# Performance work log

Hardware: AMD Instinct MI355X
Metric: run time of the kernel (lower is better)

Reference implementation:

```python
import jax, jax.numpy as jnp
import numpy as np


def setup_inputs() -> dict:
    key = jax.random.key(0)
    k1, k2, k3, k4, k5 = jax.random.split(key, 5)
    B, S, D, H, E = 4, 4096, 1024, 1024, 8  # H = per-expert hidden (fuel_dim)
    std = 0.02
    return {
        "hidden_states": jax.random.normal(k1, (B, S, D), dtype=jnp.float32),
        "gate_w": jax.random.normal(k2, (D, E), dtype=jnp.float32) * std,
        "gw": jax.random.normal(k3, (E, D, H), dtype=jnp.float32) * std,
        "pw": jax.random.normal(k4, (E, D, H), dtype=jnp.float32) * std,
        "ow": jax.random.normal(k5, (E, H, D), dtype=jnp.float32) * std,
        "top_k": 2,
    }


def reference(hidden_states, gate_w, gw, pw, ow, top_k):
    B, S, D = hidden_states.shape
    E = gate_w.shape[1]
    x = hidden_states.reshape(-1, D)  # [T, D]
    T = x.shape[0]

    # Router
    router_logits = x @ gate_w  # [T, E]
    routing_probs = jax.nn.softmax(router_logits.astype(jnp.float32), axis=-1)
    top_w, top_i = jax.lax.top_k(routing_probs, top_k)  # [T, k]
    top_w = top_w / jnp.sum(top_w, axis=-1, keepdims=True)
    top_w = top_w.astype(x.dtype)

    # Dense combine weights: zero for unselected experts -> same math as
    # the torch gather/expert/scatter loop.
    combine = jnp.zeros((T, E), dtype=x.dtype).at[
        jnp.arange(T)[:, None], top_i
    ].set(top_w)  # [T, E]

    # SwiGLU experts, batched over the expert dim.
    g = jnp.einsum('td,edh->eth', x, gw)          # [E, T, H]
    p = jnp.einsum('td,edh->eth', x, pw)          # [E, T, H]
    h = g * jax.nn.silu(p)                        # [E, T, H]
    y = jnp.einsum('eth,ehd->etd', h, ow)         # [E, T, D]
    final = jnp.einsum('etd,te->td', y, combine)  # [T, D]
    final = final.reshape(B, S, D)

    # Load-balancing loss (recomputes softmax/topk as the torch fn does)
    expert_mask = jax.nn.one_hot(top_i, E, dtype=jnp.float32)  # [T, k, E]
    tokens_per_expert = jnp.mean(expert_mask, axis=0)          # [k, E]
    router_prob_per_expert = jnp.mean(routing_probs, axis=0)   # [E]
    bl_loss = jnp.sum(tokens_per_expert * router_prob_per_expert[None, :]) * E

    return final, router_logits, bl_loss
```

## Files before the change

kernel.cpp:

```cpp
#include <hip/hip_runtime.h>
#include <hip/hip_bf16.h>
#include <cstdint>

#define T_TOK 16384
#define DDIM  1024

typedef __attribute__((ext_vector_type(8))) short bf16x8;
typedef __attribute__((ext_vector_type(4))) float f32x4;

__device__ __forceinline__ unsigned short f2bf(float f) {
  unsigned u = __builtin_bit_cast(unsigned, f);
  return (unsigned short)((u + 0x7fffu + ((u >> 16) & 1u)) >> 16);
}
__device__ __forceinline__ unsigned pk2(float a, float b) {
  return (unsigned)f2bf(a) | ((unsigned)f2bf(b) << 16);
}
__device__ __forceinline__ void gload16(const void* g, void* l) {
  typedef __attribute__((address_space(1))) const unsigned int gu32;
  typedef __attribute__((address_space(3))) unsigned int lu32;
  __builtin_amdgcn_global_load_lds((gu32*)g, (lu32*)l, 16, 0, 0);
}

__global__ __launch_bounds__(256) void convert_k(
    const float* __restrict__ gw, const float* __restrict__ pw,
    const float* __restrict__ ow, char* __restrict__ wg,
    char* __restrict__ wp, char* __restrict__ wo) {
  __shared__ float t[64][65];
  const int z = blockIdx.z;
  const int arr = z >> 3, e = z & 7;
  const float* src = (arr == 0 ? gw : arr == 1 ? pw : ow) + ((long)e << 20);
  char* dst = (arr == 0 ? wg : arr == 1 ? wp : wo) + ((long)e << 21);
  const int r0 = blockIdx.x * 64, c0 = blockIdx.y * 64;
  const int row = threadIdx.x >> 2, q = threadIdx.x & 3;
  const float4* sp = (const float4*)(src + (long)(r0 + row) * 1024 + c0 + q * 16);
  float4 v0 = sp[0], v1 = sp[1], v2 = sp[2], v3 = sp[3];
  float* tr = &t[row][q * 16];
  tr[0]=v0.x; tr[1]=v0.y; tr[2]=v0.z; tr[3]=v0.w;
  tr[4]=v1.x; tr[5]=v1.y; tr[6]=v1.z; tr[7]=v1.w;
  tr[8]=v2.x; tr[9]=v2.y; tr[10]=v2.z; tr[11]=v2.w;
  tr[12]=v3.x; tr[13]=v3.y; tr[14]=v3.z; tr[15]=v3.w;
  __syncthreads();
  const int cl = row, rq = q;
  uint4 o0, o1;
  o0.x = pk2(t[rq*16+ 0][cl], t[rq*16+ 1][cl]);
  o0.y = pk2(t[rq*16+ 2][cl], t[rq*16+ 3][cl]);
  o0.z = pk2(t[rq*16+ 4][cl], t[rq*16+ 5][cl]);
  o0.w = pk2(t[rq*16+ 6][cl], t[rq*16+ 7][cl]);
  o1.x = pk2(t[rq*16+ 8][cl], t[rq*16+ 9][cl]);
  o1.y = pk2(t[rq*16+10][cl], t[rq*16+11][cl]);
  o1.z = pk2(t[rq*16+12][cl], t[rq*16+13][cl]);
  o1.w = pk2(t[rq*16+14][cl], t[rq*16+15][cl]);
  char* dp = dst + (long)(c0 + cl) * 2048 + (long)(r0 + rq * 16) * 2;
  *(uint4*)dp = o0;
  *(uint4*)(dp + 16) = o1;
}

__global__ __launch_bounds__(256) void router_k(
    const float* __restrict__ x, const float* __restrict__ gatew,
    float* __restrict__ logitsOut, float4* __restrict__ route,
    float* __restrict__ accum, unsigned short* __restrict__ xbo) {
  __shared__ float accB[16];
  const int tid = threadIdx.x;
  if (tid < 16) accB[tid] = 0.f;
  __syncthreads();
  const int lane = tid & 63;
  const int gwave = blockIdx.x * 4 + (tid >> 6);

  for (int g = gwave; g < 4096; g += 1024) {
    const int t0 = g * 4;
    float s[4][8];
#pragma unroll
    for (int tt = 0; tt < 4; ++tt)
#pragma unroll
      for (int e = 0; e < 8; ++e) s[tt][e] = 0.f;

    for (int i = 0; i < 16; ++i) {
      int d = lane + i * 64;
      float4 w0 = *(const float4*)(gatew + d * 8);
      float4 w1 = *(const float4*)(gatew + d * 8 + 4);
#pragma unroll
      for (int tt = 0; tt < 4; ++tt) {
        float xv = x[(long)(t0 + tt) * DDIM + d];
        if (xbo) xbo[(long)(t0 + tt) * DDIM + d] = f2bf(xv);
        s[tt][0] += xv * w0.x; s[tt][1] += xv * w0.y;
        s[tt][2] += xv * w0.z; s[tt][3] += xv * w0.w;
        s[tt][4] += xv * w1.x; s[tt][5] += xv * w1.y;
        s[tt][6] += xv * w1.z; s[tt][7] += xv * w1.w;
      }
    }
#pragma unroll
    for (int m = 1; m < 64; m <<= 1)
#pragma unroll
      for (int tt = 0; tt < 4; ++tt)
#pragma unroll
        for (int e = 0; e < 8; ++e) s[tt][e] += __shfl_xor(s[tt][e], m);

    float psum[8];
#pragma unroll
    for (int e = 0; e < 8; ++e) psum[e] = 0.f;
    int i1a[4], i2a[4];
    float w1a[4], w2a[4];
#pragma unroll
    for (int tt = 0; tt < 4; ++tt) {
      float mx = s[tt][0];
#pragma unroll
      for (int e = 1; e < 8; ++e) mx = fmaxf(mx, s[tt][e]);
      float pe[8], Z = 0.f;
#pragma unroll
      for (int e = 0; e < 8; ++e) { pe[e] = __expf(s[tt][e] - mx); Z += pe[e]; }
      float inv = 1.f / Z;
#pragma unroll
      for (int e = 0; e < 8; ++e) { pe[e] *= inv; psum[e] += pe[e]; }
      int i1 = 0; float p1 = pe[0];
#pragma unroll
      for (int e = 1; e < 8; ++e) if (pe[e] > p1) { p1 = pe[e]; i1 = e; }
      int i2 = -1; float p2 = -1.f;
#pragma unroll
      for (int e = 0; e < 8; ++e)
        if (e != i1 && pe[e] > p2) { p2 = pe[e]; i2 = e; }
      float wsum = p1 + p2;
      i1a[tt] = i1; i2a[tt] = i2;
      w1a[tt] = p1 / wsum; w2a[tt] = p2 / wsum;
    }
    if (lane < 32) {
      int tt = lane >> 3, e = lane & 7;
      logitsOut[(t0 + tt) * 8 + e] = s[tt][e];
    }
    if (lane < 32 && (lane & 7) == 0) {
      int tt = lane >> 3;
      float4 rr;
      rr.x = w1a[tt]; rr.y = w2a[tt];
      rr.z = __int_as_float(i1a[tt]); rr.w = __int_as_float(i2a[tt]);
      route[t0 + tt] = rr;
    }
    if (lane < 8) {
      float c = 0.f;
#pragma unroll
      for (int tt = 0; tt < 4; ++tt)
        c += (float)(i1a[tt] == lane) + (float)(i2a[tt] == lane);
      atomicAdd(&accB[lane], psum[lane]);
      atomicAdd(&accB[8 + lane], c);
    }
  }
  __syncthreads();
  if (tid < 16) atomicAdd(&accum[tid], accB[tid]);
}

__global__ void offsets_k(const float* __restrict__ accum,
                          int* __restrict__ offs, int* __restrict__ cursor) {
  if (threadIdx.x == 0) {
    int c = 0;
#pragma unroll
    for (int e = 0; e < 8; ++e) {
      offs[e] = c; cursor[e] = c;
      c += (int)(accum[8 + e] + 0.5f);
    }
    offs[8] = c;
  }
}

__global__ __launch_bounds__(256) void scatter_k(
    const float4* __restrict__ route, int* __restrict__ cursor,
    int* __restrict__ list, float* __restrict__ wsl) {
  int t = blockIdx.x * 256 + threadIdx.x;
  float4 rr = route[t];
  int i1 = __float_as_int(rr.z), i2 = __float_as_int(rr.w);
  int s1 = atomicAdd(&cursor[i1], 1);
  list[s1] = t; wsl[s1] = rr.x;
  int s2 = atomicAdd(&cursor[i2], 1);
  list[s2] = t; wsl[s2] = rr.y;
}

template <int XB>
__global__ __launch_bounds__(512) void pass1_k(
    const float* __restrict__ x, const unsigned short* __restrict__ xb,
    const char* __restrict__ wg, const char* __restrict__ wp,
    const int* __restrict__ list, const float* __restrict__ wsl,
    const int* __restrict__ offs, char* __restrict__ hw) {
  __shared__ __align__(16) char Al[2][16384];
  __shared__ __align__(16) char Bgl[2][16384];
  __shared__ __align__(16) char Bpl[2][16384];
  const int e = blockIdx.x >> 7, tile = blockIdx.x & 127;
  const int s0 = offs[e], s1 = offs[e + 1];
  const int start = s0 + tile * 128;
  if (start >= s1) return;
  const int valid = min(128, s1 - start);
  const int chunk = blockIdx.y;
  const int tid = threadIdx.x, lane = tid & 63, wid = tid >> 6;

  const int l8 = lane >> 3, seg = lane & 7;
  const unsigned inrow = ((unsigned)(seg * 16)) ^ (((unsigned)l8) << 4);
  const int br0 = wid * 16 + l8, br1 = br0 + 8;
  const long wbase = ((long)e << 21) + ((long)(chunk * 128) << 11);
  const char* gsrc0 = wg + wbase + ((long)br0 << 11) + inrow;
  const char* gsrc1 = wg + wbase + ((long)br1 << 11) + inrow;
  const char* psrc0 = wp + wbase + ((long)br0 << 11) + inrow;
  const char* psrc1 = wp + wbase + ((long)br1 << 11) + inrow;
  const unsigned ld0 = (unsigned)(wid * 2048), ld1 = ld0 + 1024;

  const int tokA0 = list[start + min(br0, valid - 1)];
  const int tokA1 = list[start + min(br1, valid - 1)];
  const char* asrc0 = (const char*)xb + ((long)tokA0 << 11) + inrow;
  const char* asrc1 = (const char*)xb + ((long)tokA1 << 11) + inrow;
  const int sr = tid >> 2, q = tid & 3;
  const int tokS = list[start + min(sr, valid - 1)];
  const float* axp = x + (long)tokS * DDIM + q * 16;
  const unsigned swz = ((unsigned)(sr & 7)) << 4;
  const unsigned sb = (unsigned)(sr * 128 + q * 32);

  f32x4 aG[4][2], aP[4][2];
#pragma unroll
  for (int f = 0; f < 4; ++f)
#pragma unroll
    for (int j = 0; j < 2; ++j) {
      aG[f][j] = (f32x4){0.f, 0.f, 0.f, 0.f};
      aP[f][j] = (f32x4){0.f, 0.f, 0.f, 0.f};
    }

  const int col = lane & 15, kg = lane >> 4;
  const int mb = (wid >> 2) * 64, nb = (wid & 3) * 32;

#define P1_STAGE_B(kb, buf)                                   \
  {                                                           \
    long ko = (long)(kb) << 7;                                \
    gload16(gsrc0 + ko, &Bgl[buf][ld0]);                      \
    gload16(gsrc1 + ko, &Bgl[buf][ld1]);                      \
    gload16(psrc0 + ko, &Bpl[buf][ld0]);                      \
    gload16(psrc1 + ko, &Bpl[buf][ld1]);                      \
  }
#define P1_STAGE_A_XB(kb, buf)                                \
  {                                                           \
    long ko = (long)(kb) << 7;                                \
    gload16(asrc0 + ko, &Al[buf][ld0]);                       \
    gload16(asrc1 + ko, &Al[buf][ld1]);                       \
  }
#define P1_STAGE_A_F32(kb, buf)                               \
  {                                                           \
    const float4* ap = (const float4*)(axp + (kb) * 64);      \
    float4 v0 = ap[0], v1 = ap[1], v2 = ap[2], v3 = ap[3];    \
    uint4 w0, w1;                                             \
    w0.x = pk2(v0.x, v0.y); w0.y = pk2(v0.z, v0.w);           \
    w0.z = pk2(v1.x, v1.y); w0.w = pk2(v1.z, v1.w);           \
    w1.x = pk2(v2.x, v2.y); w1.y = pk2(v2.z, v2.w);           \
    w1.z = pk2(v3.x, v3.y); w1.w = pk2(v3.z, v3.w);           \
    *(uint4*)(&Al[buf][0] + (sb ^ swz)) = w0;                 \
    *(uint4*)(&Al[buf][0] + ((sb + 16) ^ swz)) = w1;          \
  }

  if (XB) P1_STAGE_A_XB(0, 0) else P1_STAGE_A_F32(0, 0);
  P1_STAGE_B(0, 0);
  __syncthreads();

  for (int kb = 0; kb < 16; ++kb) {
    const int cur = kb & 1;
    bf16x8 af[2][4], bg2[2][2], bp2[2][2];
#pragma unroll
    for (int ks = 0; ks < 2; ++ks) {
#pragma unroll
      for (int f = 0; f < 4; ++f) {
        int r = mb + f * 16 + col;
        af[ks][f] = *(const bf16x8*)(
            &Al[cur][0] + ((unsigned)(r * 128 + ks * 64 + kg * 16) ^
                           (((unsigned)r & 7u) << 4)));
      }
#pragma unroll
      for (int j = 0; j < 2; ++j) {
        int n = nb + j * 16 + col;
        unsigned off = (unsigned)(n * 128 + ks * 64 + kg * 16) ^
                       (((unsigned)n & 7u) << 4);
        bg2[ks][j] = *(const bf16x8*)(&Bgl[cur][0] + off);
        bp2[ks][j] = *(const bf16x8*)(&Bpl[cur][0] + off);
      }
    }
    if (kb < 15) {
      if (XB) P1_STAGE_A_XB(kb + 1, cur ^ 1) else P1_STAGE_A_F32(kb + 1, cur ^ 1);
      P1_STAGE_B(kb + 1, cur ^ 1);
    }
#pragma unroll
    for (int ks = 0; ks < 2; ++ks)
#pragma unroll
      for (int f = 0; f < 4; ++f)
#pragma unroll
        for (int j = 0; j < 2; ++j) {
          aG[f][j] = __builtin_amdgcn_mfma_f32_16x16x32_bf16(
              af[ks][f], bg2[ks][j], aG[f][j], 0, 0, 0);
          aP[f][j] = __builtin_amdgcn_mfma_f32_16x16x32_bf16(
              af[ks][f], bp2[ks][j], aP[f][j], 0, 0, 0);
        }
    __syncthreads();
  }

  const int rg = lane >> 4;
#pragma unroll
  for (int f = 0; f < 4; ++f) {
#pragma unroll
    for (int r = 0; r < 4; ++r) {
      int ml = mb + f * 16 + rg * 4 + r;
      if (ml < valid) {
        int slot = start + ml;
        float wv = wsl[slot];
#pragma unroll
        for (int j = 0; j < 2; ++j) {
          float g = aG[f][j][r], p = aP[f][j][r];
          float h = g * (p / (1.f + __expf(-p))) * wv;
          int hc = chunk * 128 + nb + j * 16 + col;
          *(unsigned short*)(hw + (((long)slot << 11) + (hc << 1))) = f2bf(h);
        }
      }
    }
  }
}

__global__ __launch_bounds__(512) void pass2_k(
    const char* __restrict__ hw, const char* __restrict__ wo,
    const int* __restrict__ list, const int* __restrict__ offs,
    float* __restrict__ out) {
  __shared__ __align__(16) char Al[2][16384];
  __shared__ __align__(16) char Bl[2][32768];
  const int e = blockIdx.x >> 7, tile = blockIdx.x & 127;
  const int s0 = offs[e], s1 = offs[e + 1];
  const int start = s0 + tile * 128;
  if (start >= s1) return;
  const int valid = min(128, s1 - start);
  const int chunk = blockIdx.y;
  const int tid = threadIdx.x, lane = tid & 63, wid = tid >> 6;

  const int l8 = lane >> 3, seg = lane & 7;
  const unsigned inrow = ((unsigned)(seg * 16)) ^ (((unsigned)l8) << 4);
  const int ar0 = wid * 16 + l8, ar1 = ar0 + 8;
  const char* asrc0 = hw + ((long)(start + min(ar0, valid - 1)) << 11) + inrow;
  const char* asrc1 = hw + ((long)(start + min(ar1, valid - 1)) << 11) + inrow;
  const unsigned lda0 = (unsigned)(wid * 2048), lda1 = lda0 + 1024;
  const long wobase = ((long)e << 21) + ((long)(chunk * 256) << 11);
  const char* bsrc[4];
  unsigned ldb[4];
#pragma unroll
  for (int i = 0; i < 4; ++i) {
    int n = wid * 32 + i * 8 + l8;
    bsrc[i] = wo + wobase + ((long)n << 11) + inrow;
    ldb[i] = (unsigned)(wid * 4096 + i * 1024);
  }

  f32x4 acc[4][4];
#pragma unroll
  for (int f = 0; f < 4; ++f)
#pragma unroll
    for (int j = 0; j < 4; ++j) acc[f][j] = (f32x4){0.f, 0.f, 0.f, 0.f};

  const int col = lane & 15, kg = lane >> 4;
  const int mb = (wid >> 2) * 64, nb = (wid & 3) * 64;

#define P2_STAGE(kb, buf)                                     \
  {                                                           \
    long ko = (long)(kb) << 7;                                \
    gload16(asrc0 + ko, &Al[buf][lda0]);                      \
    gload16(asrc1 + ko, &Al[buf][lda1]);                      \
    gload16(bsrc[0] + ko, &Bl[buf][ldb[0]]);                  \
    gload16(bsrc[1] + ko, &Bl[buf][ldb[1]]);                  \
    gload16(bsrc[2] + ko, &Bl[buf][ldb[2]]);                  \
    gload16(bsrc[3] + ko, &Bl[buf][ldb[3]]);                  \
  }

  P2_STAGE(0, 0);
  __syncthreads();

  for (int kb = 0; kb < 16; ++kb) {
    const int cur = kb & 1;
    bf16x8 af[2][4], bf4[2][4];
#pragma unroll
    for (int ks = 0; ks < 2; ++ks) {
#pragma unroll
      for (int f = 0; f < 4; ++f) {
        int r = mb + f * 16 + col;
        af[ks][f] = *(const bf16x8*)(
            &Al[cur][0] + ((unsigned)(r * 128 + ks * 64 + kg * 16) ^
                           (((unsigned)r & 7u) << 4)));
      }
#pragma unroll
      for (int j = 0; j < 4; ++j) {
        int n = nb + j * 16 + col;
        bf4[ks][j] = *(const bf16x8*)(
            &Bl[cur][0] + ((unsigned)(n * 128 + ks * 64 + kg * 16) ^
                           (((unsigned)n & 7u) << 4)));
      }
    }
    if (kb < 15) P2_STAGE(kb + 1, cur ^ 1);
#pragma unroll
    for (int ks = 0; ks < 2; ++ks)
#pragma unroll
      for (int f = 0; f < 4; ++f)
#pragma unroll
        for (int j = 0; j < 4; ++j)
          acc[f][j] = __builtin_amdgcn_mfma_f32_16x16x32_bf16(
              af[ks][f], bf4[ks][j], acc[f][j], 0, 0, 0);
    __syncthreads();
  }

  const int rg = lane >> 4;
#pragma unroll
  for (int f = 0; f < 4; ++f) {
#pragma unroll
    for (int r = 0; r < 4; ++r) {
      int ml = mb + f * 16 + rg * 4 + r;
      if (ml < valid) {
        int token = list[start + ml];
#pragma unroll
        for (int j = 0; j < 4; ++j) {
          int c = chunk * 256 + nb + j * 16 + col;
          atomicAdd(&out[(long)token * DDIM + c], acc[f][j][r]);
        }
      }
    }
  }
}

__global__ void loss_k(const float* __restrict__ accum, float* __restrict__ out) {
  if (threadIdx.x == 0 && blockIdx.x == 0) {
    float L = 0.f;
#pragma unroll
    for (int e = 0; e < 8; ++e) L += accum[e] * accum[8 + e];
    out[0] = L * 8.f / ((float)T_TOK * (float)T_TOK);
  }
}

extern "C" void kernel_launch(void* const* d_in, const int* in_sizes, int n_in,
                              void* d_out, int out_size, void* d_ws,
                              size_t ws_size, hipStream_t stream) {
  const float* x     = (const float*)d_in[0];
  const float* gatew = (const float*)d_in[1];
  const float* gw    = (const float*)d_in[2];
  const float* pw    = (const float*)d_in[3];
  const float* ow    = (const float*)d_in[4];

  float* out       = (float*)d_out;
  float* logitsOut = out + (long)T_TOK * DDIM;
  float* lossOut   = out + (long)T_TOK * DDIM + T_TOK * 8;

  char* wsB = (char*)d_ws;
  float*  accum  = (float*)wsB;
  int*    cursor = (int*)(wsB + 64);
  int*    offs   = (int*)(wsB + 96);
  float4* route  = (float4*)(wsB + 1024);
  int*    list   = (int*)(wsB + 263168);
  float*  wsl    = (float*)(wsB + 394240);
  char*   wg     = wsB + (1l << 20);
  char*   wp     = wsB + 17825792;
  char*   wo     = wsB + 34603008;
  char*   hw     = wsB + 51380224;
  unsigned short* xb = (unsigned short*)(wsB + 118489088);
  const bool big = ws_size >= 152043520ul;

  hipMemsetAsync(d_out, 0, (size_t)out_size * 4, stream);
  hipMemsetAsync(accum, 0, 64, stream);
  convert_k<<<dim3(16, 16, 24), 256, 0, stream>>>(gw, pw, ow, wg, wp, wo);
  router_k<<<256, 256, 0, stream>>>(x, gatew, logitsOut, route, accum,
                                    big ? xb : nullptr);
  offsets_k<<<1, 64, 0, stream>>>(accum, offs, cursor);
  scatter_k<<<64, 256, 0, stream>>>(route, cursor, list, wsl);
  if (big)
    pass1_k<1><<<dim3(1024, 8), 512, 0, stream>>>(x, xb, wg, wp, list, wsl,
                                                  offs, hw);
  else
    pass1_k<0><<<dim3(1024, 8), 512, 0, stream>>>(x, xb, wg, wp, list, wsl,
                                                  offs, hw);
  pass2_k<<<dim3(1024, 4), 512, 0, stream>>>(hw, wo, list, offs, out);
  loss_k<<<1, 64, 0, stream>>>(accum, lossOut);
}
```

Before: 737.9 us.

## Prefetch two K-blocks ahead with explicit vmcnt waits and MFMA priority

Restructures both grouped GEMM main loops so global-to-LDS loads run two stages ahead. Explicit s_waitcnt vmcnt/lgkmcnt and raw s_barrier with sched_barrier replace the per-iteration __syncthreads. MFMA blocks are wrapped in s_setprio to favour matrix issue, and the fp32-input fallback path becomes a single-buffered loop. The aim is to hide global load latency behind the MFMAs, at the risk of subtle hazards if the hand-counted vmcnt(6) does not match the outstanding loads.

```diff
diff --git a/kernel.cpp b/kernel.cpp
--- a/kernel.cpp
+++ b/kernel.cpp
@@ -20,6 +20,20 @@
   typedef __attribute__((address_space(3))) unsigned int lu32;
   __builtin_amdgcn_global_load_lds((gu32*)g, (lu32*)l, 16, 0, 0);
 }
+
+#define SBAR()                        \
+  __builtin_amdgcn_sched_barrier(0);  \
+  __builtin_amdgcn_s_barrier();       \
+  __builtin_amdgcn_sched_barrier(0)
+#define WAIT_VM6()                                        \
+  asm volatile("s_waitcnt vmcnt(6)" ::: "memory");        \
+  __builtin_amdgcn_sched_barrier(0)
+#define WAIT_VM0()                                        \
+  asm volatile("s_waitcnt vmcnt(0)" ::: "memory");        \
+  __builtin_amdgcn_sched_barrier(0)
+#define WAIT_LGKM0()                                      \
+  asm volatile("s_waitcnt lgkmcnt(0)" ::: "memory");      \
+  __builtin_amdgcn_sched_barrier(0)
 
 __global__ __launch_bounds__(256) void convert_k(
     const float* __restrict__ gw, const float* __restrict__ pw,
@@ -220,74 +234,89 @@
   const int col = lane & 15, kg = lane >> 4;
   const int mb = (wid >> 2) * 64, nb = (wid & 3) * 32;
 
-#define P1_STAGE_B(kb, buf)                                   \
+#define P1_STAGE(kb, buf)                                     \
   {                                                           \
     long ko = (long)(kb) << 7;                                \
+    gload16(asrc0 + ko, &Al[buf][ld0]);                       \
+    gload16(asrc1 + ko, &Al[buf][ld1]);                       \
     gload16(gsrc0 + ko, &Bgl[buf][ld0]);                      \
     gload16(gsrc1 + ko, &Bgl[buf][ld1]);                      \
     gload16(psrc0 + ko, &Bpl[buf][ld0]);                      \
     gload16(psrc1 + ko, &Bpl[buf][ld1]);                      \
   }
-#define P1_STAGE_A_XB(kb, buf)                                \
-  {                                                           \
-    long ko = (long)(kb) << 7;                                \
-    gload16(asrc0 + ko, &Al[buf][ld0]);                       \
-    gload16(asrc1 + ko, &Al[buf][ld1]);                       \
-  }
-#define P1_STAGE_A_F32(kb, buf)                               \
-  {                                                           \
-    const float4* ap = (const float4*)(axp + (kb) * 64);      \
-    float4 v0 = ap[0], v1 = ap[1], v2 = ap[2], v3 = ap[3];    \
-    uint4 w0, w1;                                             \
-    w0.x = pk2(v0.x, v0.y); w0.y = pk2(v0.z, v0.w);           \
-    w0.z = pk2(v1.x, v1.y); w0.w = pk2(v1.z, v1.w);           \
-    w1.x = pk2(v2.x, v2.y); w1.y = pk2(v2.z, v2.w);           \
-    w1.z = pk2(v3.x, v3.y); w1.w = pk2(v3.z, v3.w);           \
-    *(uint4*)(&Al[buf][0] + (sb ^ swz)) = w0;                 \
-    *(uint4*)(&Al[buf][0] + ((sb + 16) ^ swz)) = w1;          \
-  }
-
-  if (XB) P1_STAGE_A_XB(0, 0) else P1_STAGE_A_F32(0, 0);
-  P1_STAGE_B(0, 0);
-  __syncthreads();
-
-  for (int kb = 0; kb < 16; ++kb) {
-    const int cur = kb & 1;
-    bf16x8 af[2][4], bg2[2][2], bp2[2][2];
-#pragma unroll
-    for (int ks = 0; ks < 2; ++ks) {
-#pragma unroll
-      for (int f = 0; f < 4; ++f) {
-        int r = mb + f * 16 + col;
-        af[ks][f] = *(const bf16x8*)(
-            &Al[cur][0] + ((unsigned)(r * 128 + ks * 64 + kg * 16) ^
-                           (((unsigned)r & 7u) << 4)));
+#define P1_FRAGS(cur)                                                      \
+  bf16x8 af[2][4], bg2[2][2], bp2[2][2];                                   \
+  _Pragma("unroll") for (int ks = 0; ks < 2; ++ks) {                       \
+    _Pragma("unroll") for (int f = 0; f < 4; ++f) {                        \
+      int r = mb + f * 16 + col;                                           \
+      af[ks][f] = *(const bf16x8*)(                                        \
+          &Al[cur][0] + ((unsigned)(r * 128 + ks * 64 + kg * 16) ^         \
+                         (((unsigned)r & 7u) << 4)));                      \
+    }                                                                      \
+    _Pragma("unroll") for (int j = 0; j < 2; ++j) {                        \
+      int n = nb + j * 16 + col;                                           \
+      unsigned off = (unsigned)(n * 128 + ks * 64 + kg * 16) ^             \
+                     (((unsigned)n & 7u) << 4);                            \
+      bg2[ks][j] = *(const bf16x8*)(&Bgl[cur][0] + off);                   \
+      bp2[ks][j] = *(const bf16x8*)(&Bpl[cur][0] + off);                   \
+    }                                                                      \
+  }
+#define P1_MFMA()                                                          \
+  __builtin_amdgcn_s_setprio(1);                                           \
+  _Pragma("unroll") for (int ks = 0; ks < 2; ++ks)                         \
+  _Pragma("unroll") for (int f = 0; f < 4; ++f)                            \
+  _Pragma("unroll") for (int j = 0; j < 2; ++j) {                          \
+    aG[f][j] = __builtin_amdgcn_mfma_f32_16x16x32_bf16(                    \
+        af[ks][f], bg2[ks][j], aG[f][j], 0, 0, 0);                         \
+    aP[f][j] = __builtin_amdgcn_mfma_f32_16x16x32_bf16(                    \
+        af[ks][f], bp2[ks][j], aP[f][j], 0, 0, 0);                         \
+  }                                                                        \
+  __builtin_amdgcn_s_setprio(0)
+
+  if (XB) {
+    P1_STAGE(0, 0);
+    P1_STAGE(1, 1);
+#pragma unroll 1
+    for (int kb = 0; kb < 15; ++kb) {
+      const int cur = kb & 1;
+      WAIT_VM6();
+      SBAR();
+      P1_FRAGS(cur);
+      WAIT_LGKM0();
+      SBAR();
+      if (kb < 14) P1_STAGE(kb + 2, cur);
+      P1_MFMA();
+    }
+    {
+      WAIT_VM0();
+      SBAR();
+      P1_FRAGS(1);
+      WAIT_LGKM0();
+      P1_MFMA();
+    }
+  } else {
+    for (int kb = 0; kb < 16; ++kb) {
+      __syncthreads();
+      {
+        const float4* ap = (const float4*)(axp + kb * 64);
+        float4 v0 = ap[0], v1 = ap[1], v2 = ap[2], v3 = ap[3];
+        uint4 w0, w1;
+        w0.x = pk2(v0.x, v0.y); w0.y = pk2(v0.z, v0.w);
+        w0.z = pk2(v1.x, v1.y); w0.w = pk2(v1.z, v1.w);
+        w1.x = pk2(v2.x, v2.y); w1.y = pk2(v2.z, v2.w);
+        w1.z = pk2(v3.x, v3.y); w1.w = pk2(v3.z, v3.w);
+        *(uint4*)(&Al[0][0] + (sb ^ swz)) = w0;
+        *(uint4*)(&Al[0][0] + ((sb + 16) ^ swz)) = w1;
+        long ko = (long)kb << 7;
+        gload16(gsrc0 + ko, &Bgl[0][ld0]);
+        gload16(gsrc1 + ko, &Bgl[0][ld1]);
+        gload16(psrc0 + ko, &Bpl[0][ld0]);
+        gload16(psrc1 + ko, &Bpl[0][ld1]);
       }
-#pragma unroll
-      for (int j = 0; j < 2; ++j) {
-        int n = nb + j * 16 + col;
-        unsigned off = (unsigned)(n * 128 + ks * 64 + kg * 16) ^
-                       (((unsigned)n & 7u) << 4);
-        bg2[ks][j] = *(const bf16x8*)(&Bgl[cur][0] + off);
-        bp2[ks][j] = *(const bf16x8*)(&Bpl[cur][0] + off);
-      }
-    }
-    if (kb < 15) {
-      if (XB) P1_STAGE_A_XB(kb + 1, cur ^ 1) else P1_STAGE_A_F32(kb + 1, cur ^ 1);
-      P1_STAGE_B(kb + 1, cur ^ 1);
-    }
-#pragma unroll
-    for (int ks = 0; ks < 2; ++ks)
-#pragma unroll
-      for (int f = 0; f < 4; ++f)
-#pragma unroll
-        for (int j = 0; j < 2; ++j) {
-          aG[f][j] = __builtin_amdgcn_mfma_f32_16x16x32_bf16(
-              af[ks][f], bg2[ks][j], aG[f][j], 0, 0, 0);
-          aP[f][j] = __builtin_amdgcn_mfma_f32_16x16x32_bf16(
-              af[ks][f], bp2[ks][j], aP[f][j], 0, 0, 0);
-        }
-    __syncthreads();
+      __syncthreads();
+      P1_FRAGS(0);
+      P1_MFMA();
+    }
   }
 
   const int rg = lane >> 4;
@@ -360,40 +389,50 @@
     gload16(bsrc[2] + ko, &Bl[buf][ldb[2]]);                  \
     gload16(bsrc[3] + ko, &Bl[buf][ldb[3]]);                  \
   }
+#define P2_FRAGS(cur)                                                      \
+  bf16x8 af[2][4], bf4[2][4];                                              \
+  _Pragma("unroll") for (int ks = 0; ks < 2; ++ks) {                       \
+    _Pragma("unroll") for (int f = 0; f < 4; ++f) {                        \
+      int r = mb + f * 16 + col;                                           \
+      af[ks][f] = *(const bf16x8*)(                                        \
+          &Al[cur][0] + ((unsigned)(r * 128 + ks * 64 + kg * 16) ^         \
+                         (((unsigned)r & 7u) << 4)));                      \
+    }                                                                      \
+    _Pragma("unroll") for (int j = 0; j < 4; ++j) {                        \
+      int n = nb + j * 16 + col;                                           \
+      bf4[ks][j] = *(const bf16x8*)(                                       \
+          &Bl[cur][0] + ((unsigned)(n * 128 + ks * 64 + kg * 16) ^         \
+                         (((unsigned)n & 7u) << 4)));                      \
+    }                                                                      \
+  }
+#define P2_MFMA()                                                          \
+  __builtin_amdgcn_s_setprio(1);                                           \
+  _Pragma("unroll") for (int ks = 0; ks < 2; ++ks)                         \
+  _Pragma("unroll") for (int f = 0; f < 4; ++f)                            \
+  _Pragma("unroll") for (int j = 0; j < 4; ++j)                            \
+    acc[f][j] = __builtin_amdgcn_mfma_f32_16x16x32_bf16(                   \
+        af[ks][f], bf4[ks][j], acc[f][j], 0, 0, 0);                        \
+  __builtin_amdgcn_s_setprio(0)
 
   P2_STAGE(0, 0);
-  __syncthreads();
-
-  for (int kb = 0; kb < 16; ++kb) {
+  P2_STAGE(1, 1);
+#pragma unroll 1
+  for (int kb = 0; kb < 15; ++kb) {
     const int cur = kb & 1;
-    bf16x8 af[2][4], bf4[2][4];
-#pragma unroll
-    for (int ks = 0; ks < 2; ++ks) {
-#pragma unroll
-      for (int f = 0; f < 4; ++f) {
-        int r = mb + f * 16 + col;
-        af[ks][f] = *(const bf16x8*)(
-            &Al[cur][0] + ((unsigned)(r * 128 + ks * 64 + kg * 16) ^
-                           (((unsigned)r & 7u) << 4)));
-      }
-#pragma unroll
-      for (int j = 0; j < 4; ++j) {
-        int n = nb + j * 16 + col;
-        bf4[ks][j] = *(const bf16x8*)(
-            &Bl[cur][0] + ((unsigned)(n * 128 + ks * 64 + kg * 16) ^
-                           (((unsigned)n & 7u) << 4)));
-      }
-    }
-    if (kb < 15) P2_STAGE(kb + 1, cur ^ 1);
-#pragma unroll
-    for (int ks = 0; ks < 2; ++ks)
-#pragma unroll
-      for (int f = 0; f < 4; ++f)
-#pragma unroll
-        for (int j = 0; j < 4; ++j)
-          acc[f][j] = __builtin_amdgcn_mfma_f32_16x16x32_bf16(
-              af[ks][f], bf4[ks][j], acc[f][j], 0, 0, 0);
-    __syncthreads();
+    WAIT_VM6();
+    SBAR();
+    P2_FRAGS(cur);
+    WAIT_LGKM0();
+    SBAR();
+    if (kb < 14) P2_STAGE(kb + 2, cur);
+    P2_MFMA();
+  }
+  {
+    WAIT_VM0();
+    SBAR();
+    P2_FRAGS(1);
+    WAIT_LGKM0();
+    P2_MFMA();
   }
 
   const int rg = lane >> 4;
```

New measurement: 709.9 us. -3.8%, faster.

## Double token tile to 256 rows, interleave experts, and pipeline with explicit vmcnt waits

Applied to the files above, without the earlier changes.

Both expert GEMM kernels now cover 256 routed tokens per block instead of 128. Each wave holds 8 row fragments, so every weight tile loaded from global memory is reused across twice as many tokens. Block indices are interleaved across experts. The double-buffered loop now uses one barrier per step, partial vmcnt waits, sched barriers and setprio, so the next stage's loads overlap the MFMA work. Register pressure rises with the larger accumulators, and LDS use doubles to about 128KB in pass1, which may limit blocks per CU despite the launch_bounds hint of 2.

```diff
diff --git a/kernel.cpp b/kernel.cpp
--- a/kernel.cpp
+++ b/kernel.cpp
@@ -20,6 +20,17 @@
   typedef __attribute__((address_space(3))) unsigned int lu32;
   __builtin_amdgcn_global_load_lds((gu32*)g, (lu32*)l, 16, 0, 0);
 }
+
+#define SBAR()                        \
+  __builtin_amdgcn_sched_barrier(0);  \
+  __builtin_amdgcn_s_barrier();       \
+  __builtin_amdgcn_sched_barrier(0)
+#define WAIT_VM8()                                        \
+  asm volatile("s_waitcnt vmcnt(8)" ::: "memory");        \
+  __builtin_amdgcn_sched_barrier(0)
+#define WAIT_VM0()                                        \
+  asm volatile("s_waitcnt vmcnt(0)" ::: "memory");        \
+  __builtin_amdgcn_sched_barrier(0)
 
 __global__ __launch_bounds__(256) void convert_k(
     const float* __restrict__ gw, const float* __restrict__ pw,
@@ -172,45 +183,49 @@
 }
 
 template <int XB>
-__global__ __launch_bounds__(512) void pass1_k(
+__global__ __launch_bounds__(512, 2) void pass1_k(
     const float* __restrict__ x, const unsigned short* __restrict__ xb,
     const char* __restrict__ wg, const char* __restrict__ wp,
     const int* __restrict__ list, const float* __restrict__ wsl,
     const int* __restrict__ offs, char* __restrict__ hw) {
-  __shared__ __align__(16) char Al[2][16384];
+  __shared__ __align__(16) char Al[2][32768];
   __shared__ __align__(16) char Bgl[2][16384];
   __shared__ __align__(16) char Bpl[2][16384];
-  const int e = blockIdx.x >> 7, tile = blockIdx.x & 127;
+  const int e = blockIdx.x & 7, tile = blockIdx.x >> 3;
   const int s0 = offs[e], s1 = offs[e + 1];
-  const int start = s0 + tile * 128;
+  const int start = s0 + tile * 256;
   if (start >= s1) return;
-  const int valid = min(128, s1 - start);
+  const int valid = min(256, s1 - start);
   const int chunk = blockIdx.y;
   const int tid = threadIdx.x, lane = tid & 63, wid = tid >> 6;
 
   const int l8 = lane >> 3, seg = lane & 7;
   const unsigned inrow = ((unsigned)(seg * 16)) ^ (((unsigned)l8) << 4);
-  const int br0 = wid * 16 + l8, br1 = br0 + 8;
+
+  const char* asrc[4];
+  unsigned adst[4];
+#pragma unroll
+  for (int i = 0; i < 4; ++i) {
+    int row = wid * 32 + i * 8 + l8;
+    int tok = list[start + min(row, valid - 1)];
+    asrc[i] = (const char*)xb + ((long)tok << 11) + inrow;
+    adst[i] = (unsigned)(wid * 4096 + i * 1024);
+  }
   const long wbase = ((long)e << 21) + ((long)(chunk * 128) << 11);
-  const char* gsrc0 = wg + wbase + ((long)br0 << 11) + inrow;
-  const char* gsrc1 = wg + wbase + ((long)br1 << 11) + inrow;
-  const char* psrc0 = wp + wbase + ((long)br0 << 11) + inrow;
-  const char* psrc1 = wp + wbase + ((long)br1 << 11) + inrow;
-  const unsigned ld0 = (unsigned)(wid * 2048), ld1 = ld0 + 1024;
-
-  const int tokA0 = list[start + min(br0, valid - 1)];
-  const int tokA1 = list[start + min(br1, valid - 1)];
-  const char* asrc0 = (const char*)xb + ((long)tokA0 << 11) + inrow;
-  const char* asrc1 = (const char*)xb + ((long)tokA1 << 11) + inrow;
-  const int sr = tid >> 2, q = tid & 3;
-  const int tokS = list[start + min(sr, valid - 1)];
-  const float* axp = x + (long)tokS * DDIM + q * 16;
-  const unsigned swz = ((unsigned)(sr & 7)) << 4;
-  const unsigned sb = (unsigned)(sr * 128 + q * 32);
-
-  f32x4 aG[4][2], aP[4][2];
-#pragma unroll
-  for (int f = 0; f < 4; ++f)
+  const char* gsrc[2];
+  const char* psrc[2];
+  unsigned bdst[2];
+#pragma unroll
+  for (int i = 0; i < 2; ++i) {
+    int h = wid * 16 + i * 8 + l8;
+    gsrc[i] = wg + wbase + ((long)h << 11) + inrow;
+    psrc[i] = wp + wbase + ((long)h << 11) + inrow;
+    bdst[i] = (unsigned)(wid * 2048 + i * 1024);
+  }
+
+  f32x4 aG[8][2], aP[8][2];
+#pragma unroll
+  for (int f = 0; f < 8; ++f)
 #pragma unroll
     for (int j = 0; j < 2; ++j) {
       aG[f][j] = (f32x4){0.f, 0.f, 0.f, 0.f};
@@ -218,81 +233,92 @@
     }
 
   const int col = lane & 15, kg = lane >> 4;
-  const int mb = (wid >> 2) * 64, nb = (wid & 3) * 32;
-
-#define P1_STAGE_B(kb, buf)                                   \
+  const int mb = (wid >> 2) * 128, nb = (wid & 3) * 32;
+
+#define P1_STAGE(kb, buf)                                     \
   {                                                           \
     long ko = (long)(kb) << 7;                                \
-    gload16(gsrc0 + ko, &Bgl[buf][ld0]);                      \
-    gload16(gsrc1 + ko, &Bgl[buf][ld1]);                      \
-    gload16(psrc0 + ko, &Bpl[buf][ld0]);                      \
-    gload16(psrc1 + ko, &Bpl[buf][ld1]);                      \
-  }
-#define P1_STAGE_A_XB(kb, buf)                                \
-  {                                                           \
-    long ko = (long)(kb) << 7;                                \
-    gload16(asrc0 + ko, &Al[buf][ld0]);                       \
-    gload16(asrc1 + ko, &Al[buf][ld1]);                       \
-  }
-#define P1_STAGE_A_F32(kb, buf)                               \
-  {                                                           \
-    const float4* ap = (const float4*)(axp + (kb) * 64);      \
-    float4 v0 = ap[0], v1 = ap[1], v2 = ap[2], v3 = ap[3];    \
-    uint4 w0, w1;                                             \
-    w0.x = pk2(v0.x, v0.y); w0.y = pk2(v0.z, v0.w);           \
-    w0.z = pk2(v1.x, v1.y); w0.w = pk2(v1.z, v1.w);           \
-    w1.x = pk2(v2.x, v2.y); w1.y = pk2(v2.z, v2.w);           \
-    w1.z = pk2(v3.x, v3.y); w1.w = pk2(v3.z, v3.w);           \
-    *(uint4*)(&Al[buf][0] + (sb ^ swz)) = w0;                 \
-    *(uint4*)(&Al[buf][0] + ((sb + 16) ^ swz)) = w1;          \
-  }
-
-  if (XB) P1_STAGE_A_XB(0, 0) else P1_STAGE_A_F32(0, 0);
-  P1_STAGE_B(0, 0);
-  __syncthreads();
-
-  for (int kb = 0; kb < 16; ++kb) {
-    const int cur = kb & 1;
-    bf16x8 af[2][4], bg2[2][2], bp2[2][2];
-#pragma unroll
-    for (int ks = 0; ks < 2; ++ks) {
-#pragma unroll
-      for (int f = 0; f < 4; ++f) {
-        int r = mb + f * 16 + col;
-        af[ks][f] = *(const bf16x8*)(
-            &Al[cur][0] + ((unsigned)(r * 128 + ks * 64 + kg * 16) ^
-                           (((unsigned)r & 7u) << 4)));
-      }
-#pragma unroll
-      for (int j = 0; j < 2; ++j) {
-        int n = nb + j * 16 + col;
-        unsigned off = (unsigned)(n * 128 + ks * 64 + kg * 16) ^
-                       (((unsigned)n & 7u) << 4);
-        bg2[ks][j] = *(const bf16x8*)(&Bgl[cur][0] + off);
-        bp2[ks][j] = *(const bf16x8*)(&Bpl[cur][0] + off);
-      }
-    }
-    if (kb < 15) {
-      if (XB) P1_STAGE_A_XB(kb + 1, cur ^ 1) else P1_STAGE_A_F32(kb + 1, cur ^ 1);
-      P1_STAGE_B(kb + 1, cur ^ 1);
-    }
-#pragma unroll
-    for (int ks = 0; ks < 2; ++ks)
-#pragma unroll
-      for (int f = 0; f < 4; ++f)
-#pragma unroll
-        for (int j = 0; j < 2; ++j) {
-          aG[f][j] = __builtin_amdgcn_mfma_f32_16x16x32_bf16(
-              af[ks][f], bg2[ks][j], aG[f][j], 0, 0, 0);
-          aP[f][j] = __builtin_amdgcn_mfma_f32_16x16x32_bf16(
-              af[ks][f], bp2[ks][j], aP[f][j], 0, 0, 0);
+    gload16(asrc[0] + ko, &Al[buf][adst[0]]);                 \
+    gload16(asrc[1] + ko, &Al[buf][adst[1]]);                 \
+    gload16(asrc[2] + ko, &Al[buf][adst[2]]);                 \
+    gload16(asrc[3] + ko, &Al[buf][adst[3]]);                 \
+    gload16(gsrc[0] + ko, &Bgl[buf][bdst[0]]);                \
+    gload16(gsrc[1] + ko, &Bgl[buf][bdst[1]]);                \
+    gload16(psrc[0] + ko, &Bpl[buf][bdst[0]]);                \
+    gload16(psrc[1] + ko, &Bpl[buf][bdst[1]]);                \
+  }
+#define P1_COMPUTE(cur)                                                     \
+  _Pragma("unroll") for (int ks = 0; ks < 2; ++ks) {                        \
+    bf16x8 bg[2], bp[2];                                                    \
+    _Pragma("unroll") for (int j = 0; j < 2; ++j) {                         \
+      int n = nb + j * 16 + col;                                            \
+      unsigned off = (unsigned)(n * 128 + ks * 64 + kg * 16) ^              \
+                     (((unsigned)n & 7u) << 4);                             \
+      bg[j] = *(const bf16x8*)(&Bgl[cur][0] + off);                         \
+      bp[j] = *(const bf16x8*)(&Bpl[cur][0] + off);                         \
+    }                                                                       \
+    _Pragma("unroll") for (int f = 0; f < 8; ++f) {                         \
+      int r = mb + f * 16 + col;                                            \
+      bf16x8 a = *(const bf16x8*)(                                          \
+          &Al[cur][0] + ((unsigned)(r * 128 + ks * 64 + kg * 16) ^          \
+                         (((unsigned)r & 7u) << 4)));                       \
+      _Pragma("unroll") for (int j = 0; j < 2; ++j) {                       \
+        aG[f][j] = __builtin_amdgcn_mfma_f32_16x16x32_bf16(a, bg[j],        \
+                                                           aG[f][j], 0, 0, 0); \
+        aP[f][j] = __builtin_amdgcn_mfma_f32_16x16x32_bf16(a, bp[j],        \
+                                                           aP[f][j], 0, 0, 0); \
+      }                                                                     \
+    }                                                                       \
+  }
+
+  if (XB) {
+    P1_STAGE(0, 0);
+#pragma unroll 1
+    for (int kb = 0; kb < 16; ++kb) {
+      const int cur = kb & 1;
+      SBAR();
+      if (kb < 15) {
+        P1_STAGE(kb + 1, cur ^ 1);
+        WAIT_VM8();
+      } else {
+        WAIT_VM0();
+      }
+      __builtin_amdgcn_s_setprio(1);
+      P1_COMPUTE(cur);
+      __builtin_amdgcn_s_setprio(0);
+    }
+  } else {
+    const int sr2 = tid >> 1, q2 = tid & 1;
+    const int tokS = list[start + min(sr2, valid - 1)];
+    const float* axp = x + (long)tokS * DDIM + q2 * 32;
+    const unsigned swzS = ((unsigned)(sr2 & 7)) << 4;
+    const unsigned sbS = (unsigned)(sr2 * 128 + q2 * 64);
+    for (int kb = 0; kb < 16; ++kb) {
+      __syncthreads();
+      {
+        const float4* ap = (const float4*)(axp + kb * 64);
+#pragma unroll
+        for (int m = 0; m < 4; ++m) {
+          float4 v0 = ap[m * 2], v1 = ap[m * 2 + 1];
+          uint4 w;
+          w.x = pk2(v0.x, v0.y); w.y = pk2(v0.z, v0.w);
+          w.z = pk2(v1.x, v1.y); w.w = pk2(v1.z, v1.w);
+          *(uint4*)(&Al[0][0] + ((sbS + m * 16) ^ swzS)) = w;
         }
-    __syncthreads();
+        long ko = (long)kb << 7;
+        gload16(gsrc[0] + ko, &Bgl[0][bdst[0]]);
+        gload16(gsrc[1] + ko, &Bgl[0][bdst[1]]);
+        gload16(psrc[0] + ko, &Bpl[0][bdst[0]]);
+        gload16(psrc[1] + ko, &Bpl[0][bdst[1]]);
+      }
+      __syncthreads();
+      P1_COMPUTE(0);
+    }
   }
 
   const int rg = lane >> 4;
 #pragma unroll
-  for (int f = 0; f < 4; ++f) {
+  for (int f = 0; f < 8; ++f) {
 #pragma unroll
     for (int r = 0; r < 4; ++r) {
       int ml = mb + f * 16 + rg * 4 + r;
@@ -311,94 +337,97 @@
   }
 }
 
-__global__ __launch_bounds__(512) void pass2_k(
+__global__ __launch_bounds__(512, 2) void pass2_k(
     const char* __restrict__ hw, const char* __restrict__ wo,
     const int* __restrict__ list, const int* __restrict__ offs,
     float* __restrict__ out) {
-  __shared__ __align__(16) char Al[2][16384];
+  __shared__ __align__(16) char Al[2][32768];
   __shared__ __align__(16) char Bl[2][32768];
-  const int e = blockIdx.x >> 7, tile = blockIdx.x & 127;
+  const int e = blockIdx.x & 7, tile = blockIdx.x >> 3;
   const int s0 = offs[e], s1 = offs[e + 1];
-  const int start = s0 + tile * 128;
+  const int start = s0 + tile * 256;
   if (start >= s1) return;
-  const int valid = min(128, s1 - start);
+  const int valid = min(256, s1 - start);
   const int chunk = blockIdx.y;
   const int tid = threadIdx.x, lane = tid & 63, wid = tid >> 6;
 
   const int l8 = lane >> 3, seg = lane & 7;
   const unsigned inrow = ((unsigned)(seg * 16)) ^ (((unsigned)l8) << 4);
-  const int ar0 = wid * 16 + l8, ar1 = ar0 + 8;
-  const char* asrc0 = hw + ((long)(start + min(ar0, valid - 1)) << 11) + inrow;
-  const char* asrc1 = hw + ((long)(start + min(ar1, valid - 1)) << 11) + inrow;
-  const unsigned lda0 = (unsigned)(wid * 2048), lda1 = lda0 + 1024;
-  const long wobase = ((long)e << 21) + ((long)(chunk * 256) << 11);
+
+  const char* asrc[4];
   const char* bsrc[4];
-  unsigned ldb[4];
+  unsigned dst4[4];
 #pragma unroll
   for (int i = 0; i < 4; ++i) {
+    int row = wid * 32 + i * 8 + l8;
+    asrc[i] = hw + ((long)(start + min(row, valid - 1)) << 11) + inrow;
     int n = wid * 32 + i * 8 + l8;
-    bsrc[i] = wo + wobase + ((long)n << 11) + inrow;
-    ldb[i] = (unsigned)(wid * 4096 + i * 1024);
-  }
-
-  f32x4 acc[4][4];
-#pragma unroll
-  for (int f = 0; f < 4; ++f)
+    bsrc[i] = wo + ((long)e << 21) + ((long)(chunk * 256 + n) << 11) + inrow;
+    dst4[i] = (unsigned)(wid * 4096 + i * 1024);
+  }
+
+  f32x4 acc[8][4];
+#pragma unroll
+  for (int f = 0; f < 8; ++f)
 #pragma unroll
     for (int j = 0; j < 4; ++j) acc[f][j] = (f32x4){0.f, 0.f, 0.f, 0.f};
 
   const int col = lane & 15, kg = lane >> 4;
-  const int mb = (wid >> 2) * 64, nb = (wid & 3) * 64;
+  const int mb = (wid >> 2) * 128, nb = (wid & 3) * 64;
 
 #define P2_STAGE(kb, buf)                                     \
   {                                                           \
     long ko = (long)(kb) << 7;                                \
-    gload16(asrc0 + ko, &Al[buf][lda0]);                      \
-    gload16(asrc1 + ko, &Al[buf][lda1]);                      \
-    gload16(bsrc[0] + ko, &Bl[buf][ldb[0]]);                  \
-    gload16(bsrc[1] + ko, &Bl[buf][ldb[1]]);                  \
-    gload16(bsrc[2] + ko, &Bl[buf][ldb[2]]);                  \
-    gload16(bsrc[3] + ko, &Bl[buf][ldb[3]]);                  \
+    gload16(asrc[0] + ko, &Al[buf][dst4[0]]);                 \
+    gload16(asrc[1] + ko, &Al[buf][dst4[1]]);                 \
+    gload16(asrc[2] + ko, &Al[buf][dst4[2]]);                 \
+    gload16(asrc[3] + ko, &Al[buf][dst4[3]]);                 \
+    gload16(bsrc[0] + ko, &Bl[buf][dst4[0]]);                 \
+    gload16(bsrc[1] + ko, &Bl[buf][dst4[1]]);                 \
+    gload16(bsrc[2] + ko, &Bl[buf][dst4[2]]);                 \
+    gload16(bsrc[3] + ko, &Bl[buf][dst4[3]]);                 \
   }
 
   P2_STAGE(0, 0);
-  __syncthreads();
-
+#pragma unroll 1
   for (int kb = 0; kb < 16; ++kb) {
     const int cur = kb & 1;
-    bf16x8 af[2][4], bf4[2][4];
+    SBAR();
+    if (kb < 15) {
+      P2_STAGE(kb + 1, cur ^ 1);
+      WAIT_VM8();
+    } else {
+      WAIT_VM0();
+    }
+    __builtin_amdgcn_s_setprio(1);
 #pragma unroll
     for (int ks = 0; ks < 2; ++ks) {
-#pragma unroll
-      for (int f = 0; f < 4; ++f) {
+      bf16x8 bf4[4];
+#pragma unroll
+      for (int j = 0; j < 4; ++j) {
+        int n = nb + j * 16 + col;
+        bf4[j] = *(const bf16x8*)(
+            &Bl[cur][0] + ((unsigned)(n * 128 + ks * 64 + kg * 16) ^
+                           (((unsigned)n & 7u) << 4)));
+      }
+#pragma unroll
+      for (int f = 0; f < 8; ++f) {
         int r = mb + f * 16 + col;
-        af[ks][f] = *(const bf16x8*)(
+        bf16x8 a = *(const bf16x8*)(
             &Al[cur][0] + ((unsigned)(r * 128 + ks * 64 + kg * 16) ^
                            (((unsigned)r & 7u) << 4)));
-      }
-#pragma unroll
-      for (int j = 0; j < 4; ++j) {
-        int n = nb + j * 16 + col;
-        bf4[ks][j] = *(const bf16x8*)(
-            &Bl[cur][0] + ((unsigned)(n * 128 + ks * 64 + kg * 16) ^
-                           (((unsigned)n & 7u) << 4)));
-      }
-    }
-    if (kb < 15) P2_STAGE(kb + 1, cur ^ 1);
-#pragma unroll
-    for (int ks = 0; ks < 2; ++ks)
-#pragma unroll
-      for (int f = 0; f < 4; ++f)
 #pragma unroll
         for (int j = 0; j < 4; ++j)
-          acc[f][j] = __builtin_amdgcn_mfma_f32_16x16x32_bf16(
-              af[ks][f], bf4[ks][j], acc[f][j], 0, 0, 0);
-    __syncthreads();
+          acc[f][j] = __builtin_amdgcn_mfma_f32_16x16x32_bf16(a, bf4[j],
+                                                              acc[f][j], 0, 0, 0);
+      }
+    }
+    __builtin_amdgcn_s_setprio(0);
   }
 
   const int rg = lane >> 4;
 #pragma unroll
-  for (int f = 0; f < 4; ++f) {
+  for (int f = 0; f < 8; ++f) {
 #pragma unroll
     for (int r = 0; r < 4; ++r) {
       int ml = mb + f * 16 + rg * 4 + r;
@@ -458,11 +487,11 @@
   offsets_k<<<1, 64, 0, stream>>>(accum, offs, cursor);
   scatter_k<<<64, 256, 0, stream>>>(route, cursor, list, wsl);
   if (big)
-    pass1_k<1><<<dim3(1024, 8), 512, 0, stream>>>(x, xb, wg, wp, list, wsl,
-                                                  offs, hw);
+    pass1_k<1><<<dim3(512, 8), 512, 0, stream>>>(x, xb, wg, wp, list, wsl,
+                                                 offs, hw);
   else
-    pass1_k<0><<<dim3(1024, 8), 512, 0, stream>>>(x, xb, wg, wp, list, wsl,
-                                                  offs, hw);
-  pass2_k<<<dim3(1024, 4), 512, 0, stream>>>(hw, wo, list, offs, out);
+    pass1_k<0><<<dim3(512, 8), 512, 0, stream>>>(x, xb, wg, wp, list, wsl,
+                                                 offs, hw);
+  pass2_k<<<dim3(512, 4), 512, 0, stream>>>(hw, wo, list, offs, out);
   loss_k<<<1, 64, 0, stream>>>(accum, lossOut);
 }
```

After: 694.9 us. -5.8%, faster.
